# Kernel optimization log

Hardware: AMD Instinct MI355X
Metric: run time of the kernel (lower is better)

## Reference

```python
import jax, jax.numpy as jnp
import numpy as np

KERNEL = 3  # 2*half_size + 1 with half_size=1
ITER = 20


def _pool(v):
    # MaxPool2d(kernel=3, stride=1, padding=1) == SAME max reduce_window on NCHW
    return jax.lax.reduce_window(v, -jnp.inf, jax.lax.max,
                                 (1, 1, KERNEL, KERNEL), (1, 1, 1, 1), 'SAME')


def _erode(v):
    return -_pool(-v)


def setup_inputs() -> dict:
    key = jax.random.key(0)
    x = jax.random.normal(key, (16, 1, 1024, 1024), dtype=jnp.float32)
    return {"x": x}


def reference(x):
    skel0 = x - _pool(_erode(x))  # open(x) = dilate(erode(x))

    def step(carry, _):
        xc, skel = carry
        xc = _erode(xc)
        skel = skel + (xc - _pool(_erode(xc)))
        return (xc, skel), None

    (_, skel), _ = jax.lax.scan(step, (x, skel0), None, length=ITER)
    return skel
```

## Files before the change

kernel.cpp:

```cpp
#include <hip/hip_runtime.h>


static constexpr int W = 1024, H = 1024, NIMG = 16;
static constexpr int RCH = 32;
static constexpr int NSTEP = RCH + 16;
static constexpr float BIG = 3.0e38f;

__device__ __forceinline__ float min3f(float a, float b, float c) { return fminf(fminf(a, b), c); }
__device__ __forceinline__ float max3f(float a, float b, float c) { return fmaxf(fmaxf(a, b), c); }

template<bool FIRST, bool WRITE_E, int PFI>
__device__ __forceinline__
void pipe_step(int t, int y0, int lane, int gx,
               bool leftEdge, bool rightEdge, bool lane_ok,
               const float* __restrict__ in, float* __restrict__ eo,
               float* __restrict__ sk,
               float4 (&OB)[7], float4 (&MB)[7], float4& OD, float4& MD,
               float4 (&acc)[8], float4 (&pf)[2], float4 (&skpf)[2])
{
    float4 cur;
    if ((unsigned)t < (unsigned)H) cur = pf[PFI];
    else                           cur = make_float4(BIG, BIG, BIG, BIG);
    {
        const int nr = t + 2;
        if ((unsigned)nr < (unsigned)H && nr <= y0 + RCH + 7)
            pf[PFI] = *(const float4*)&in[(size_t)nr * W + gx];
    }

#pragma unroll
    for (int s = 0; s < 7; ++s) {
        const float4 fOld = OB[s];
        const float4 fMid = MB[s];

        float4 vm;
        vm.x = min3f(fOld.x, fMid.x, cur.x);
        vm.y = min3f(fOld.y, fMid.y, cur.y);
        vm.z = min3f(fOld.z, fMid.z, cur.z);
        vm.w = min3f(fOld.w, fMid.w, cur.w);
        float lft = __shfl(vm.w, lane - 1);
        float rgt = __shfl(vm.x, lane + 1);
        if (leftEdge)  lft = BIG;
        if (rightEdge) rgt = BIG;
        float4 en;
        en.x = min3f(lft,  vm.x, vm.y);
        en.y = min3f(vm.x, vm.y, vm.z);
        en.z = min3f(vm.y, vm.z, vm.w);
        en.w = min3f(vm.z, vm.w, rgt);

        OB[s] = cur;

        float4 gOld, gMid;
        if (s < 6) { gOld = OB[s + 1]; gMid = MB[s + 1]; }
        else       { gOld = OD;        gMid = MD;        }
        const bool topOK = (t - s - 3) >= 0;
        const bool botOK = (t - s - 1) < H;
        float4 vx;
        {
            float txx = topOK ? gOld.x : -BIG, bxx = botOK ? en.x : -BIG;
            float txy = topOK ? gOld.y : -BIG, bxy = botOK ? en.y : -BIG;
            float txz = topOK ? gOld.z : -BIG, bxz = botOK ? en.z : -BIG;
            float txw = topOK ? gOld.w : -BIG, bxw = botOK ? en.w : -BIG;
            vx.x = max3f(txx, gMid.x, bxx);
            vx.y = max3f(txy, gMid.y, bxy);
            vx.z = max3f(txz, gMid.z, bxz);
            vx.w = max3f(txw, gMid.w, bxw);
        }
        float dl = __shfl(vx.w, lane - 1);
        float dr = __shfl(vx.x, lane + 1);
        if (leftEdge)  dl = -BIG;
        if (rightEdge) dr = -BIG;
        float4 dn;
        dn.x = max3f(dl,   vx.x, vx.y);
        dn.y = max3f(vx.x, vx.y, vx.z);
        dn.z = max3f(vx.y, vx.z, vx.w);
        dn.w = max3f(vx.z, vx.w, dr);

        acc[6 - s].x += fOld.x - dn.x;
        acc[6 - s].y += fOld.y - dn.y;
        acc[6 - s].z += fOld.z - dn.z;
        acc[6 - s].w += fOld.w - dn.w;

        if (s == 6) {
            if (WRITE_E) {
                const int er = t - 7;
                if (er >= y0 && er < y0 + RCH && lane_ok)
                    *(float4*)&eo[(size_t)er * W + gx] = en;
            }
            OD = en;
        }
        cur = en;
    }

    if (t >= y0 + 8) {
        const int r = t - 8;
        float4 v = acc[0];
        if (!FIRST) {
            const float4 o = skpf[PFI];
            v.x += o.x; v.y += o.y; v.z += o.z; v.w += o.w;
        }
        if (lane_ok)
            *(float4*)&sk[(size_t)r * W + gx] = v;
    }
#pragma unroll
    for (int j = 0; j < 7; ++j) acc[j] = acc[j + 1];
    acc[7] = make_float4(0.f, 0.f, 0.f, 0.f);

    if (!FIRST) {
        const int pr = t - 6;
        if (pr >= y0 && pr < y0 + RCH)
            skpf[PFI] = *(const float4*)&sk[(size_t)pr * W + gx];
    }
}

template<bool FIRST, bool WRITE_E>
__global__ __launch_bounds__(64)
void skel_pipe(const float* __restrict__ ein, float* __restrict__ eout,
               float* __restrict__ skel)
{
    const int lane = threadIdx.x;
    const int bx = blockIdx.x;
    const int y0 = blockIdx.y * RCH;
    const int img = blockIdx.z;
    const int x0 = (bx == 4) ? 768 : bx * 240;
    const int gx = x0 + 4 * lane;

    const size_t base = (size_t)img * (size_t)(W * H);
    const float* __restrict__ in = ein + base;
    float* __restrict__ eo = eout + base;
    float* __restrict__ sk = skel + base;

    const bool leftEdge  = (gx == 0);
    const bool rightEdge = (gx + 4 == W);
    const int own_lo = (bx == 0) ? 0 : ((bx == 4) ? 968 : x0 + 8);
    const int own_hi = (bx == 4) ? W : x0 + 248;
    const bool lane_ok = (gx >= own_lo) && (gx < own_hi);

    float4 B0[7], B1[7], D0, D1, acc[8], pf[2], skpf[2];
    const float4 big4 = make_float4(BIG, BIG, BIG, BIG);
    const float4 z4   = make_float4(0.f, 0.f, 0.f, 0.f);
#pragma unroll
    for (int s = 0; s < 7; ++s) { B0[s] = big4; B1[s] = big4; }
    D0 = big4; D1 = big4;
#pragma unroll
    for (int j = 0; j < 8; ++j) acc[j] = z4;
    pf[0] = big4; pf[1] = big4; skpf[0] = z4; skpf[1] = z4;

    {
        const int r0 = y0 - 8, r1 = y0 - 7;
        if (r0 >= 0) pf[0] = *(const float4*)&in[(size_t)r0 * W + gx];
        if (r1 >= 0) pf[1] = *(const float4*)&in[(size_t)r1 * W + gx];
    }

    const int t0 = y0 - 8;
#pragma unroll 1
    for (int t = t0; t < t0 + NSTEP; t += 2) {
        pipe_step<FIRST, WRITE_E, 0>(t,     y0, lane, gx, leftEdge, rightEdge, lane_ok,
                                     in, eo, sk, B0, B1, D0, D1, acc, pf, skpf);
        pipe_step<FIRST, WRITE_E, 1>(t + 1, y0, lane, gx, leftEdge, rightEdge, lane_ok,
                                     in, eo, sk, B1, B0, D1, D0, acc, pf, skpf);
    }
}

extern "C" void kernel_launch(void* const* d_in, const int* in_sizes, int n_in,
                              void* d_out, int out_size, void* d_ws, size_t ws_size,
                              hipStream_t stream)
{
    const float* x = (const float*)d_in[0];
    float* skel = (float*)d_out;
    const size_t n = (size_t)NIMG * W * H;

    float* e0 = (float*)d_ws;
    float* e1 = e0 + n;

    dim3 grid(5, H / RCH, NIMG);
    dim3 block(64);

    skel_pipe<true,  true ><<<grid, block, 0, stream>>>(x,  e0, skel);
    skel_pipe<false, true ><<<grid, block, 0, stream>>>(e0, e1, skel);
    skel_pipe<false, false><<<grid, block, 0, stream>>>(e1, e0, skel);
}
```

Baseline: 373.1 us.

## Share one neighbor shuffle per row between erosion and opening dilation

Reorders the per-stage pipeline so the dilation for each opening runs on the previous stage's eroded rows. Each new row is shuffled once to get its left and right neighbor values, which are cached in per-stage halo registers and reused for both the vertical-min erosion and the vertical-max dilation. This replaces two shuffles of intermediate results per stage, cutting cross-lane traffic roughly in half. In exchange it adds four 8-entry float register arrays, which raise register pressure and could lower occupancy, and it shifts the accumulator indexing by one stage.

```diff
diff --git a/kernel.cpp b/kernel.cpp
--- a/kernel.cpp
+++ b/kernel.cpp
@@ -16,6 +16,7 @@
                const float* __restrict__ in, float* __restrict__ eo,
                float* __restrict__ sk,
                float4 (&OB)[7], float4 (&MB)[7], float4& OD, float4& MD,
+               float (&hLo)[8], float (&hLn)[8], float (&hRo)[8], float (&hRn)[8],
                float4 (&acc)[8], float4 (&pf)[2], float4 (&skpf)[2])
 {
     float4 cur;
@@ -27,68 +28,93 @@
             pf[PFI] = *(const float4*)&in[(size_t)nr * W + gx];
     }
 
+    float4 keep;
+
 #pragma unroll
     for (int s = 0; s < 7; ++s) {
         const float4 fOld = OB[s];
         const float4 fMid = MB[s];
+
+        const float nL = __shfl(cur.w, lane - 1);
+        const float nR = __shfl(cur.x, lane + 1);
+
+        if (s >= 1) {
+            const bool topOK = (t - s - 2) >= 0;
+            const bool botOK = (t - s) < H;
+            float4 vx;
+            vx.x = max3f(topOK ? fOld.x : -BIG, fMid.x, botOK ? cur.x : -BIG);
+            vx.y = max3f(topOK ? fOld.y : -BIG, fMid.y, botOK ? cur.y : -BIG);
+            vx.z = max3f(topOK ? fOld.z : -BIG, fMid.z, botOK ? cur.z : -BIG);
+            vx.w = max3f(topOK ? fOld.w : -BIG, fMid.w, botOK ? cur.w : -BIG);
+            float vxL = max3f(topOK ? hLo[s] : -BIG, hLn[s], botOK ? nL : -BIG);
+            float vxR = max3f(topOK ? hRo[s] : -BIG, hRn[s], botOK ? nR : -BIG);
+            if (leftEdge)  vxL = -BIG;
+            if (rightEdge) vxR = -BIG;
+            float4 dn;
+            dn.x = max3f(vxL,  vx.x, vx.y);
+            dn.y = max3f(vx.x, vx.y, vx.z);
+            dn.z = max3f(vx.y, vx.z, vx.w);
+            dn.w = max3f(vx.z, vx.w, vxR);
+            acc[7 - s].x += keep.x - dn.x;
+            acc[7 - s].y += keep.y - dn.y;
+            acc[7 - s].z += keep.z - dn.z;
+            acc[7 - s].w += keep.w - dn.w;
+        }
 
         float4 vm;
         vm.x = min3f(fOld.x, fMid.x, cur.x);
         vm.y = min3f(fOld.y, fMid.y, cur.y);
         vm.z = min3f(fOld.z, fMid.z, cur.z);
         vm.w = min3f(fOld.w, fMid.w, cur.w);
-        float lft = __shfl(vm.w, lane - 1);
-        float rgt = __shfl(vm.x, lane + 1);
-        if (leftEdge)  lft = BIG;
-        if (rightEdge) rgt = BIG;
+        float vmL = min3f(hLo[s], hLn[s], nL);
+        float vmR = min3f(hRo[s], hRn[s], nR);
+        if (leftEdge)  vmL = BIG;
+        if (rightEdge) vmR = BIG;
         float4 en;
-        en.x = min3f(lft,  vm.x, vm.y);
+        en.x = min3f(vmL,  vm.x, vm.y);
         en.y = min3f(vm.x, vm.y, vm.z);
         en.z = min3f(vm.y, vm.z, vm.w);
-        en.w = min3f(vm.z, vm.w, rgt);
-
-        OB[s] = cur;
-
-        float4 gOld, gMid;
-        if (s < 6) { gOld = OB[s + 1]; gMid = MB[s + 1]; }
-        else       { gOld = OD;        gMid = MD;        }
-        const bool topOK = (t - s - 3) >= 0;
-        const bool botOK = (t - s - 1) < H;
+        en.w = min3f(vm.z, vm.w, vmR);
+
+        if (s == 6 && WRITE_E) {
+            const int er = t - 7;
+            if (er >= y0 && er < y0 + RCH && lane_ok)
+                *(float4*)&eo[(size_t)er * W + gx] = en;
+        }
+
+        keep   = fOld;
+        OB[s]  = cur;
+        hLo[s] = nL;
+        hRo[s] = nR;
+        cur = en;
+    }
+
+    {
+        const float nL7 = __shfl(cur.w, lane - 1);
+        const float nR7 = __shfl(cur.x, lane + 1);
+        const bool topOK = (t - 9) >= 0;
+        const bool botOK = (t - 7) < H;
         float4 vx;
-        {
-            float txx = topOK ? gOld.x : -BIG, bxx = botOK ? en.x : -BIG;
-            float txy = topOK ? gOld.y : -BIG, bxy = botOK ? en.y : -BIG;
-            float txz = topOK ? gOld.z : -BIG, bxz = botOK ? en.z : -BIG;
-            float txw = topOK ? gOld.w : -BIG, bxw = botOK ? en.w : -BIG;
-            vx.x = max3f(txx, gMid.x, bxx);
-            vx.y = max3f(txy, gMid.y, bxy);
-            vx.z = max3f(txz, gMid.z, bxz);
-            vx.w = max3f(txw, gMid.w, bxw);
-        }
-        float dl = __shfl(vx.w, lane - 1);
-        float dr = __shfl(vx.x, lane + 1);
-        if (leftEdge)  dl = -BIG;
-        if (rightEdge) dr = -BIG;
+        vx.x = max3f(topOK ? OD.x : -BIG, MD.x, botOK ? cur.x : -BIG);
+        vx.y = max3f(topOK ? OD.y : -BIG, MD.y, botOK ? cur.y : -BIG);
+        vx.z = max3f(topOK ? OD.z : -BIG, MD.z, botOK ? cur.z : -BIG);
+        vx.w = max3f(topOK ? OD.w : -BIG, MD.w, botOK ? cur.w : -BIG);
+        float vxL = max3f(topOK ? hLo[7] : -BIG, hLn[7], botOK ? nL7 : -BIG);
+        float vxR = max3f(topOK ? hRo[7] : -BIG, hRn[7], botOK ? nR7 : -BIG);
+        if (leftEdge)  vxL = -BIG;
+        if (rightEdge) vxR = -BIG;
         float4 dn;
-        dn.x = max3f(dl,   vx.x, vx.y);
+        dn.x = max3f(vxL,  vx.x, vx.y);
         dn.y = max3f(vx.x, vx.y, vx.z);
         dn.z = max3f(vx.y, vx.z, vx.w);
-        dn.w = max3f(vx.z, vx.w, dr);
-
-        acc[6 - s].x += fOld.x - dn.x;
-        acc[6 - s].y += fOld.y - dn.y;
-        acc[6 - s].z += fOld.z - dn.z;
-        acc[6 - s].w += fOld.w - dn.w;
-
-        if (s == 6) {
-            if (WRITE_E) {
-                const int er = t - 7;
-                if (er >= y0 && er < y0 + RCH && lane_ok)
-                    *(float4*)&eo[(size_t)er * W + gx] = en;
-            }
-            OD = en;
-        }
-        cur = en;
+        dn.w = max3f(vx.z, vx.w, vxR);
+        acc[0].x += keep.x - dn.x;
+        acc[0].y += keep.y - dn.y;
+        acc[0].z += keep.z - dn.z;
+        acc[0].w += keep.w - dn.w;
+        OD     = cur;
+        hLo[7] = nL7;
+        hRo[7] = nR7;
     }
 
     if (t >= y0 + 8) {
@@ -136,11 +162,14 @@
     const bool lane_ok = (gx >= own_lo) && (gx < own_hi);
 
     float4 B0[7], B1[7], D0, D1, acc[8], pf[2], skpf[2];
+    float hA_L[8], hB_L[8], hA_R[8], hB_R[8];
     const float4 big4 = make_float4(BIG, BIG, BIG, BIG);
     const float4 z4   = make_float4(0.f, 0.f, 0.f, 0.f);
 #pragma unroll
     for (int s = 0; s < 7; ++s) { B0[s] = big4; B1[s] = big4; }
     D0 = big4; D1 = big4;
+#pragma unroll
+    for (int s = 0; s < 8; ++s) { hA_L[s] = BIG; hB_L[s] = BIG; hA_R[s] = BIG; hB_R[s] = BIG; }
 #pragma unroll
     for (int j = 0; j < 8; ++j) acc[j] = z4;
     pf[0] = big4; pf[1] = big4; skpf[0] = z4; skpf[1] = z4;
@@ -155,9 +184,11 @@
 #pragma unroll 1
     for (int t = t0; t < t0 + NSTEP; t += 2) {
         pipe_step<FIRST, WRITE_E, 0>(t,     y0, lane, gx, leftEdge, rightEdge, lane_ok,
-                                     in, eo, sk, B0, B1, D0, D1, acc, pf, skpf);
+                                     in, eo, sk, B0, B1, D0, D1,
+                                     hA_L, hB_L, hA_R, hB_R, acc, pf, skpf);
         pipe_step<FIRST, WRITE_E, 1>(t + 1, y0, lane, gx, leftEdge, rightEdge, lane_ok,
-                                     in, eo, sk, B1, B0, D1, D0, acc, pf, skpf);
+                                     in, eo, sk, B1, B0, D1, D0,
+                                     hB_L, hA_L, hB_R, hA_R, acc, pf, skpf);
     }
 }
 
```

Result: slower. 483.5 us (+29.6%).
